# Optimization experiments

Hardware: AMD Instinct MI355X
Metric: run time of the kernel (lower is better)

The kernel has to match this reference:

```python
import jax, jax.numpy as jnp
import numpy as np

N = 100000
E = 1600000
DIM = 128
HID = 16
HEADS = 4
NUM_CLASSES = 2
NEG_SLOPE = 0.2


def _glorot(key, shape):
    fan_in, fan_out = shape[0], shape[-1]
    lim = jnp.sqrt(6.0 / (fan_in + fan_out))
    return jax.random.uniform(key, shape, jnp.float32, -lim, lim)


def setup_inputs() -> dict:
    key = jax.random.key(0)
    ks = jax.random.split(key, 12)
    x = jax.random.normal(ks[0], (N, DIM), jnp.float32)
    edge_index = jax.random.randint(ks[1], (2, E), 0, N, jnp.int32)
    # conv1: in=DIM, out=HID, heads=HEADS
    W1 = _glorot(ks[2], (DIM, HEADS * HID))
    att_src1 = _glorot(ks[3], (HEADS, HID))
    att_dst1 = _glorot(ks[4], (HEADS, HID))
    b1 = jnp.zeros((HEADS * HID,), jnp.float32)
    # conv2: in=HEADS*HID, out=NUM_CLASSES, heads=1
    W2 = _glorot(ks[5], (HEADS * HID, NUM_CLASSES))
    att_src2 = _glorot(ks[6], (1, NUM_CLASSES))
    att_dst2 = _glorot(ks[7], (1, NUM_CLASSES))
    b2 = jnp.zeros((NUM_CLASSES,), jnp.float32)
    return {"x": x, "edge_index": edge_index, "W1": W1, "att_src1": att_src1,
            "att_dst1": att_dst1, "b1": b1, "W2": W2, "att_src2": att_src2,
            "att_dst2": att_dst2, "b2": b2}


def gat_conv(x, src, dst, W, a_src, a_dst, bias, heads, out_ch):
    n = x.shape[0]
    h = (x @ W).reshape(n, heads, out_ch)                      # [N,H,C]
    alpha_s = jnp.sum(h * a_src[None], axis=-1)                # [N,H]
    alpha_d = jnp.sum(h * a_dst[None], axis=-1)                # [N,H]
    e = alpha_s[src] + alpha_d[dst]                            # [Etot,H]
    e = jnp.where(e > 0, e, NEG_SLOPE * e)                     # leaky_relu
    m = jax.ops.segment_max(e, dst, num_segments=n)            # segment softmax
    e = jnp.exp(e - m[dst])
    s = jax.ops.segment_sum(e, dst, num_segments=n)
    alpha = e / (s[dst] + 1e-16)                               # [Etot,H]
    msg = h[src] * alpha[..., None]                            # [Etot,H,C]
    out = jax.ops.segment_sum(msg, dst, num_segments=n)        # [N,H,C]
    return out.reshape(n, heads * out_ch) + bias


def reference(x, edge_index, W1, att_src1, att_dst1, b1, W2, att_src2, att_dst2, b2):
    n = x.shape[0]
    loops = jnp.arange(n, dtype=edge_index.dtype)
    src = jnp.concatenate([edge_index[0], loops])
    dst = jnp.concatenate([edge_index[1], loops])
    # dropout p=0.6 is identity in eval mode
    h = gat_conv(x, src, dst, W1, att_src1, att_dst1, b1, HEADS, HID)
    h = jax.nn.elu(h)
    out = gat_conv(h, src, dst, W2, att_src2, att_dst2, b2, 1, NUM_CLASSES)
    return out
```

## Files before the change

### kernel.cpp

```cpp
#include <hip/hip_runtime.h>
#include <math.h>


#define NB 256
#define BSH 9
#define SRC_MASK 0x1FFFF
#define KC_CHUNK 4096
#define MAXB 12288

static __device__ __forceinline__ unsigned short f2bf(float f) {
    union { float f; unsigned int u; } v; v.f = f;
    unsigned int r = (v.u + 0x7fffu + ((v.u >> 16) & 1u)) >> 16;
    return (unsigned short)r;
}
static __device__ __forceinline__ float bf2f(unsigned short s) {
    union { unsigned int u; float f; } v; v.u = ((unsigned int)s) << 16;
    return v.f;
}
static __device__ __forceinline__ float lrexp(float raw) {
    return __expf(raw > 0.f ? raw : 0.2f * raw);
}

__global__ __launch_bounds__(256) void k_gemm1(const float* __restrict__ x,
                                               const float* __restrict__ W,
                                               const float* __restrict__ att_s,
                                               const float* __restrict__ att_d,
                                               unsigned short* __restrict__ h1b,
                                               float* __restrict__ as1,
                                               float* __restrict__ ad1, int n) {
    __shared__ float xs[64 * 132];
    __shared__ float Ws[128 * 64];
    const int t = threadIdx.x;
    const int row0 = blockIdx.x * 64;
    for (int i = t; i < 2048; i += 256)
        ((float4*)Ws)[i] = ((const float4*)W)[i];
    for (int i = t; i < 2048; i += 256) {
        int r = i >> 5, k4 = i & 31;
        float4 v = make_float4(0.f, 0.f, 0.f, 0.f);
        if (row0 + r < n) v = ((const float4*)x)[(size_t)(row0 + r) * 32 + k4];
        *(float4*)&xs[r * 132 + k4 * 4] = v;
    }
    __syncthreads();
    const int tx = t & 15, ty = t >> 4;
    float acc[4][4] = {};
    for (int k = 0; k < 128; k += 4) {
        float4 av[4], bv[4];
#pragma unroll
        for (int i = 0; i < 4; ++i) av[i] = *(const float4*)&xs[(ty * 4 + i) * 132 + k];
#pragma unroll
        for (int kk = 0; kk < 4; ++kk) bv[kk] = *(const float4*)&Ws[(k + kk) * 64 + tx * 4];
#pragma unroll
        for (int kk = 0; kk < 4; ++kk) {
            float4 b = bv[kk];
#pragma unroll
            for (int i = 0; i < 4; ++i) {
                float a = ((const float*)&av[i])[kk];
                acc[i][0] += a * b.x; acc[i][1] += a * b.y;
                acc[i][2] += a * b.z; acc[i][3] += a * b.w;
            }
        }
    }
    float4 sv = ((const float4*)att_s)[tx];
    float4 dv = ((const float4*)att_d)[tx];
    float ps[4], pd[4];
#pragma unroll
    for (int i = 0; i < 4; ++i) {
        ps[i] = acc[i][0] * sv.x + acc[i][1] * sv.y + acc[i][2] * sv.z + acc[i][3] * sv.w;
        pd[i] = acc[i][0] * dv.x + acc[i][1] * dv.y + acc[i][2] * dv.z + acc[i][3] * dv.w;
        int r = row0 + ty * 4 + i;
        if (r < n) {
            ushort4 b;
            b.x = f2bf(acc[i][0]); b.y = f2bf(acc[i][1]);
            b.z = f2bf(acc[i][2]); b.w = f2bf(acc[i][3]);
            ((ushort4*)h1b)[(size_t)r * 16 + tx] = b;
        }
    }
    __syncthreads();
    float* redA = xs;
    float* redB = xs + 1024;
#pragma unroll
    for (int i = 0; i < 4; ++i) {
        int row = ty * 4 + i;
        redA[row * 16 + tx] = ps[i];
        redB[row * 16 + tx] = pd[i];
    }
    __syncthreads();
    {
        int row = t >> 2, h = t & 3;
        int r = row0 + row;
        if (r < n) {
            const float* pa = &redA[row * 16 + h * 4];
            const float* pb = &redB[row * 16 + h * 4];
            as1[r * 4 + h] = pa[0] + pa[1] + pa[2] + pa[3];
            ad1[r * 4 + h] = pb[0] + pb[1] + pb[2] + pb[3];
        }
    }
}

__global__ __launch_bounds__(256) void kA_hist(const int* __restrict__ dst,
                                               int* __restrict__ bcount, int E) {
    __shared__ int h[NB];
    int t = threadIdx.x;
    h[t] = 0; __syncthreads();
    int base = blockIdx.x * KC_CHUNK;
#pragma unroll
    for (int k = 0; k < 16; ++k) {
        int i = base + k * 256 + t;
        if (i < E) atomicAdd(&h[dst[i] >> BSH], 1);
    }
    __syncthreads();
    if (h[t]) atomicAdd(&bcount[t], h[t]);
}

__global__ __launch_bounds__(256) void kB_scan(const int* __restrict__ bcount,
                                               int* __restrict__ boffs,
                                               int* __restrict__ bcursor,
                                               int* __restrict__ offs, int n, int E) {
    __shared__ int sm[NB];
    int t = threadIdx.x;
    int v = bcount[t];
    sm[t] = v; __syncthreads();
    for (int o = 1; o < NB; o <<= 1) {
        int xv = (t >= o) ? sm[t - o] : 0;
        __syncthreads();
        sm[t] += xv; __syncthreads();
    }
    boffs[t + 1] = sm[t];
    bcursor[t] = sm[t] - v;
    if (t == 0) { boffs[0] = 0; offs[n] = E; }
}

__global__ __launch_bounds__(256) void kC_bin(const int* __restrict__ src,
                                              const int* __restrict__ dst,
                                              int* __restrict__ bcursor,
                                              unsigned int* __restrict__ staged, int E) {
    __shared__ unsigned int pairs[KC_CHUNK];
    __shared__ unsigned char binOf[KC_CHUNK];
    __shared__ int h[NB], lofs[NB], lcur[NB], gbase[NB];
    int t = threadIdx.x;
    int base = blockIdx.x * KC_CHUNK;
    int cnt = E - base; if (cnt > KC_CHUNK) cnt = KC_CHUNK;
    h[t] = 0; __syncthreads();
    unsigned int myV[16]; int myBin[16];
#pragma unroll
    for (int k = 0; k < 16; ++k) {
        int li = k * 256 + t;
        myBin[k] = -1;
        if (li < cnt) {
            int gi = base + li;
            int s = src[gi], d = dst[gi];
            int bin = d >> BSH;
            myV[k] = ((unsigned int)(d & ((1 << BSH) - 1)) << 17) | (unsigned int)s;
            myBin[k] = bin;
            atomicAdd(&h[bin], 1);
        }
    }
    __syncthreads();
    int hv = h[t];
    lofs[t] = hv; __syncthreads();
    for (int o = 1; o < NB; o <<= 1) {
        int xv = (t >= o) ? lofs[t - o] : 0;
        __syncthreads();
        lofs[t] += xv; __syncthreads();
    }
    int excl = lofs[t] - hv;
    if (hv) gbase[t] = atomicAdd(&bcursor[t], hv);
    __syncthreads();
    lofs[t] = excl; lcur[t] = excl;
    __syncthreads();
#pragma unroll
    for (int k = 0; k < 16; ++k) {
        if (myBin[k] >= 0) {
            int p = atomicAdd(&lcur[myBin[k]], 1);
            pairs[p] = myV[k];
            binOf[p] = (unsigned char)myBin[k];
        }
    }
    __syncthreads();
    for (int i = t; i < cnt; i += 256) {
        int b = binOf[i];
        staged[gbase[b] + (i - lofs[b])] = pairs[i];
    }
}

__global__ __launch_bounds__(256) void kD_group(const unsigned int* __restrict__ staged,
                                                const int* __restrict__ boffs,
                                                unsigned int* __restrict__ grouped,
                                                int* __restrict__ offs, int n) {
    __shared__ int lh[512], lofs2[512], lcur2[512];
    __shared__ unsigned int st[MAXB];
    int t = threadIdx.x;
    int b = blockIdx.x;
    int base = boffs[b];
    int cnt = boffs[b + 1] - base;
    lh[t] = 0; lh[t + 256] = 0;
    __syncthreads();
    for (int i = t; i < cnt; i += 256)
        atomicAdd(&lh[staged[base + i] >> 17], 1);
    __syncthreads();
    int a0 = lh[2 * t], a1 = lh[2 * t + 1];
    int sp = a0 + a1;
    lcur2[t] = sp; __syncthreads();
    for (int o = 1; o < NB; o <<= 1) {
        int xv = (t >= o) ? lcur2[t - o] : 0;
        __syncthreads();
        lcur2[t] += xv; __syncthreads();
    }
    int excl = lcur2[t] - sp;
    lofs2[2 * t] = excl; lofs2[2 * t + 1] = excl + a0;
    __syncthreads();
#pragma unroll
    for (int q = 0; q < 2; ++q) {
        int dl = t + q * 256;
        int d = (b << BSH) + dl;
        if (d < n) offs[d] = base + lofs2[dl];
        lcur2[dl] = lofs2[dl];
    }
    __syncthreads();
    for (int i = t; i < cnt; i += 256) {
        unsigned int v = staged[base + i];
        int p = atomicAdd(&lcur2[v >> 17], 1);
        st[p] = v;
    }
    __syncthreads();
    for (int i = t; i < cnt; i += 256)
        grouped[base + i] = st[i];
}

__global__ __launch_bounds__(256) void k_agg1(
        const int* __restrict__ offs, const unsigned int* __restrict__ grouped,
        const unsigned short* __restrict__ h1b, const float* __restrict__ as1,
        const float* __restrict__ ad1, const float* __restrict__ b1,
        float* __restrict__ out1, int n) {
    const int lane = threadIdx.x & 63;
    const int d = blockIdx.x * 4 + (threadIdx.x >> 6);
    if (d >= n) return;
    const int c = lane;
    const int h = lane >> 4;
    const int sub = lane & 15;
    const int off0 = offs[d], off1 = offs[d + 1];
    const int total = off1 - off0 + 1;
    const float adh = ad1[d * 4 + h];
    const float wselfv = lrexp(as1[d * 4 + h] + adh);

    float acc = 0.f, wsum = 0.f;
    for (int base = 0; base < total; base += 16) {
        int e = base + sub;
        float w = 0.f; int s = d;
        if (e < total) {
            if (e < total - 1) {
                unsigned int v = grouped[off0 + e];
                s = (int)(v & SRC_MASK);
                w = lrexp(as1[s * 4 + h] + adh);
            } else {
                w = wselfv;
            }
        }
        wsum += w;
#pragma unroll
        for (int j = 0; j < 16; ++j) {
            int sj = __builtin_amdgcn_readlane(s, j);
            float wj = __shfl(w, (h << 4) + j);
            acc += wj * bf2f(h1b[(size_t)sj * 64 + c]);
        }
    }
    wsum += __shfl_xor(wsum, 1);
    wsum += __shfl_xor(wsum, 2);
    wsum += __shfl_xor(wsum, 4);
    wsum += __shfl_xor(wsum, 8);
    out1[(size_t)d * 64 + c] = acc / (wsum + 1e-16f) + b1[c];
}

__global__ void k_node2(const float* __restrict__ out1, const float* __restrict__ W2,
                        const float* __restrict__ att_s2, const float* __restrict__ att_d2,
                        float4* __restrict__ pack, int n) {
    int i = blockIdx.x * blockDim.x + threadIdx.x;
    if (i >= n) return;
    const float4* row = (const float4*)(out1 + (size_t)i * 64);
    float h0 = 0.f, h1v = 0.f;
#pragma unroll
    for (int q = 0; q < 16; ++q) {
        float4 v = row[q];
        float e0 = v.x > 0.f ? v.x : expm1f(v.x);
        float e1 = v.y > 0.f ? v.y : expm1f(v.y);
        float e2 = v.z > 0.f ? v.z : expm1f(v.z);
        float e3 = v.w > 0.f ? v.w : expm1f(v.w);
        int k = q * 4;
        h0  += e0 * W2[(k + 0) * 2 + 0] + e1 * W2[(k + 1) * 2 + 0]
             + e2 * W2[(k + 2) * 2 + 0] + e3 * W2[(k + 3) * 2 + 0];
        h1v += e0 * W2[(k + 0) * 2 + 1] + e1 * W2[(k + 1) * 2 + 1]
             + e2 * W2[(k + 2) * 2 + 1] + e3 * W2[(k + 3) * 2 + 1];
    }
    pack[i] = make_float4(h0, h1v,
                          h0 * att_s2[0] + h1v * att_s2[1],
                          h0 * att_d2[0] + h1v * att_d2[1]);
}

__global__ __launch_bounds__(256) void k_agg2(
        const int* __restrict__ offs, const unsigned int* __restrict__ grouped,
        const float4* __restrict__ pack, const float* __restrict__ b2,
        float* __restrict__ out, int n) {
    int t = threadIdx.x;
    int g = blockIdx.x * 16 + (t >> 4);
    int sub = t & 15;
    if (g >= n) return;
    int off0 = offs[g], off1 = offs[g + 1];
    int total = off1 - off0 + 1;
    float ad = pack[g].w;
    float a0 = 0.f, a1 = 0.f, ws = 0.f;
    for (int e = sub; e < total; e += 16) {
        int s = (e == total - 1) ? g : (int)(grouped[off0 + e] & SRC_MASK);
        float4 ps = pack[s];
        float w = lrexp(ps.z + ad);
        a0 += w * ps.x; a1 += w * ps.y; ws += w;
    }
#pragma unroll
    for (int m = 1; m < 16; m <<= 1) {
        a0 += __shfl_xor(a0, m);
        a1 += __shfl_xor(a1, m);
        ws += __shfl_xor(ws, m);
    }
    if (sub == 0) {
        float inv = 1.f / (ws + 1e-16f);
        out[(size_t)g * 2 + 0] = a0 * inv + b2[0];
        out[(size_t)g * 2 + 1] = a1 * inv + b2[1];
    }
}

extern "C" void kernel_launch(void* const* d_in, const int* in_sizes, int n_in,
                              void* d_out, int out_size, void* d_ws, size_t ws_size,
                              hipStream_t stream) {
    const float* x    = (const float*)d_in[0];
    const int*   ei   = (const int*)d_in[1];
    const float* W1   = (const float*)d_in[2];
    const float* as1w = (const float*)d_in[3];
    const float* ad1w = (const float*)d_in[4];
    const float* b1   = (const float*)d_in[5];
    const float* W2   = (const float*)d_in[6];
    const float* as2w = (const float*)d_in[7];
    const float* ad2w = (const float*)d_in[8];
    const float* b2   = (const float*)d_in[9];
    const int n = in_sizes[0] / 128;
    const int E = in_sizes[1] / 2;
    float* out = (float*)d_out;

    char* ws = (char*)d_ws;
    size_t off = 0;
    auto alloc = [&](size_t bytes) {
        void* p = ws + off;
        off = (off + bytes + 255) & ~(size_t)255;
        return p;
    };
    float*  out1   = (float*)alloc((size_t)n * 64 * 4);
    unsigned short* h1b = (unsigned short*)alloc((size_t)n * 64 * 2);
    float*  as1    = (float*)alloc((size_t)n * 4 * 4);
    float*  ad1    = (float*)alloc((size_t)n * 4 * 4);
    float4* pack   = (float4*)alloc((size_t)n * 16);
    int*    offs   = (int*)alloc((size_t)(n + 1) * 4);
    int*    bcount = (int*)alloc(NB * 4);
    int*    boffs  = (int*)alloc((NB + 1) * 4);
    int*    bcursor= (int*)alloc(NB * 4);
    unsigned int* staged  = (unsigned int*)alloc((size_t)E * 4);
    unsigned int* grouped = (unsigned int*)alloc((size_t)E * 4);

    hipMemsetAsync(bcount, 0, NB * 4, stream);

    const int nblk = (E + KC_CHUNK - 1) / KC_CHUNK;
    k_gemm1<<<(n + 63) / 64, 256, 0, stream>>>(x, W1, as1w, ad1w, h1b, as1, ad1, n);
    kA_hist<<<nblk, 256, 0, stream>>>(ei + E, bcount, E);
    kB_scan<<<1, 256, 0, stream>>>(bcount, boffs, bcursor, offs, n, E);
    kC_bin<<<nblk, 256, 0, stream>>>(ei, ei + E, bcursor, staged, E);
    kD_group<<<NB, 256, 0, stream>>>(staged, boffs, grouped, offs, n);
    k_agg1<<<(n + 3) / 4, 256, 0, stream>>>(offs, grouped, h1b, as1, ad1, b1, out1, n);
    k_node2<<<(n + 255) / 256, 256, 0, stream>>>(out1, W2, as2w, ad2w, pack, n);
    k_agg2<<<(n + 15) / 16, 256, 0, stream>>>(offs, grouped, pack, b2, out, n);
}
```

Measured before the change: 260.4 us.

## Drop histogram and scan passes with fixed-capacity bins; fuse ELU+GEMM2 into agg1

Each destination bin now gets a fixed slot of MAXB entries, so the separate histogram and scan kernels go away and kC_bin takes its bin cursor directly from a zeroed counter. kD_group writes a per-node count array in place of a global prefix offset. The layer-2 node transform (ELU, 64x2 matvec, attention logits) moves into the tail of k_agg1 through a wave-wide shuffle reduction, which removes the out1 round trip and one launch. The cost is that a bin holding more than MAXB edges would overflow, and the shuffle reduction adds work to every wave of agg1.

```diff
diff --git a/kernel.cpp b/kernel.cpp
--- a/kernel.cpp
+++ b/kernel.cpp
@@ -97,39 +97,6 @@
     }
 }
 
-__global__ __launch_bounds__(256) void kA_hist(const int* __restrict__ dst,
-                                               int* __restrict__ bcount, int E) {
-    __shared__ int h[NB];
-    int t = threadIdx.x;
-    h[t] = 0; __syncthreads();
-    int base = blockIdx.x * KC_CHUNK;
-#pragma unroll
-    for (int k = 0; k < 16; ++k) {
-        int i = base + k * 256 + t;
-        if (i < E) atomicAdd(&h[dst[i] >> BSH], 1);
-    }
-    __syncthreads();
-    if (h[t]) atomicAdd(&bcount[t], h[t]);
-}
-
-__global__ __launch_bounds__(256) void kB_scan(const int* __restrict__ bcount,
-                                               int* __restrict__ boffs,
-                                               int* __restrict__ bcursor,
-                                               int* __restrict__ offs, int n, int E) {
-    __shared__ int sm[NB];
-    int t = threadIdx.x;
-    int v = bcount[t];
-    sm[t] = v; __syncthreads();
-    for (int o = 1; o < NB; o <<= 1) {
-        int xv = (t >= o) ? sm[t - o] : 0;
-        __syncthreads();
-        sm[t] += xv; __syncthreads();
-    }
-    boffs[t + 1] = sm[t];
-    bcursor[t] = sm[t] - v;
-    if (t == 0) { boffs[0] = 0; offs[n] = E; }
-}
-
 __global__ __launch_bounds__(256) void kC_bin(const int* __restrict__ src,
                                               const int* __restrict__ dst,
                                               int* __restrict__ bcursor,
@@ -164,7 +131,7 @@
         lofs[t] += xv; __syncthreads();
     }
     int excl = lofs[t] - hv;
-    if (hv) gbase[t] = atomicAdd(&bcursor[t], hv);
+    if (hv) gbase[t] = t * MAXB + atomicAdd(&bcursor[t], hv);
     __syncthreads();
     lofs[t] = excl; lcur[t] = excl;
     __syncthreads();
@@ -184,15 +151,16 @@
 }
 
 __global__ __launch_bounds__(256) void kD_group(const unsigned int* __restrict__ staged,
-                                                const int* __restrict__ boffs,
+                                                const int* __restrict__ bcursor,
                                                 unsigned int* __restrict__ grouped,
-                                                int* __restrict__ offs, int n) {
+                                                int* __restrict__ offs,
+                                                int* __restrict__ dcnt, int n) {
     __shared__ int lh[512], lofs2[512], lcur2[512];
     __shared__ unsigned int st[MAXB];
     int t = threadIdx.x;
     int b = blockIdx.x;
-    int base = boffs[b];
-    int cnt = boffs[b + 1] - base;
+    int base = b * MAXB;
+    int cnt = bcursor[b];
     lh[t] = 0; lh[t + 256] = 0;
     __syncthreads();
     for (int i = t; i < cnt; i += 256)
@@ -213,7 +181,10 @@
     for (int q = 0; q < 2; ++q) {
         int dl = t + q * 256;
         int d = (b << BSH) + dl;
-        if (d < n) offs[d] = base + lofs2[dl];
+        if (d < n) {
+            offs[d] = base + lofs2[dl];
+            dcnt[d] = lh[dl];
+        }
         lcur2[dl] = lofs2[dl];
     }
     __syncthreads();
@@ -228,18 +199,21 @@
 }
 
 __global__ __launch_bounds__(256) void k_agg1(
-        const int* __restrict__ offs, const unsigned int* __restrict__ grouped,
+        const int* __restrict__ offs, const int* __restrict__ dcnt,
+        const unsigned int* __restrict__ grouped,
         const unsigned short* __restrict__ h1b, const float* __restrict__ as1,
         const float* __restrict__ ad1, const float* __restrict__ b1,
-        float* __restrict__ out1, int n) {
+        const float* __restrict__ W2,
+        const float* __restrict__ att_s2, const float* __restrict__ att_d2,
+        float4* __restrict__ pack, int n) {
     const int lane = threadIdx.x & 63;
     const int d = blockIdx.x * 4 + (threadIdx.x >> 6);
     if (d >= n) return;
     const int c = lane;
     const int h = lane >> 4;
     const int sub = lane & 15;
-    const int off0 = offs[d], off1 = offs[d + 1];
-    const int total = off1 - off0 + 1;
+    const int off0 = offs[d];
+    const int total = dcnt[d] + 1;
     const float adh = ad1[d * 4 + h];
     const float wselfv = lrexp(as1[d * 4 + h] + adh);
 
@@ -268,44 +242,33 @@
     wsum += __shfl_xor(wsum, 2);
     wsum += __shfl_xor(wsum, 4);
     wsum += __shfl_xor(wsum, 8);
-    out1[(size_t)d * 64 + c] = acc / (wsum + 1e-16f) + b1[c];
-}
-
-__global__ void k_node2(const float* __restrict__ out1, const float* __restrict__ W2,
-                        const float* __restrict__ att_s2, const float* __restrict__ att_d2,
-                        float4* __restrict__ pack, int n) {
-    int i = blockIdx.x * blockDim.x + threadIdx.x;
-    if (i >= n) return;
-    const float4* row = (const float4*)(out1 + (size_t)i * 64);
-    float h0 = 0.f, h1v = 0.f;
-#pragma unroll
-    for (int q = 0; q < 16; ++q) {
-        float4 v = row[q];
-        float e0 = v.x > 0.f ? v.x : expm1f(v.x);
-        float e1 = v.y > 0.f ? v.y : expm1f(v.y);
-        float e2 = v.z > 0.f ? v.z : expm1f(v.z);
-        float e3 = v.w > 0.f ? v.w : expm1f(v.w);
-        int k = q * 4;
-        h0  += e0 * W2[(k + 0) * 2 + 0] + e1 * W2[(k + 1) * 2 + 0]
-             + e2 * W2[(k + 2) * 2 + 0] + e3 * W2[(k + 3) * 2 + 0];
-        h1v += e0 * W2[(k + 0) * 2 + 1] + e1 * W2[(k + 1) * 2 + 1]
-             + e2 * W2[(k + 2) * 2 + 1] + e3 * W2[(k + 3) * 2 + 1];
-    }
-    pack[i] = make_float4(h0, h1v,
-                          h0 * att_s2[0] + h1v * att_s2[1],
-                          h0 * att_d2[0] + h1v * att_d2[1]);
+    float o1 = acc / (wsum + 1e-16f) + b1[c];
+    float o = o1 > 0.f ? o1 : expm1f(o1);
+    float2 wv = ((const float2*)W2)[c];
+    float p0 = o * wv.x, p1 = o * wv.y;
+#pragma unroll
+    for (int m = 1; m < 64; m <<= 1) {
+        p0 += __shfl_xor(p0, m);
+        p1 += __shfl_xor(p1, m);
+    }
+    if (lane == 0) {
+        pack[d] = make_float4(p0, p1,
+                              p0 * att_s2[0] + p1 * att_s2[1],
+                              p0 * att_d2[0] + p1 * att_d2[1]);
+    }
 }
 
 __global__ __launch_bounds__(256) void k_agg2(
-        const int* __restrict__ offs, const unsigned int* __restrict__ grouped,
+        const int* __restrict__ offs, const int* __restrict__ dcnt,
+        const unsigned int* __restrict__ grouped,
         const float4* __restrict__ pack, const float* __restrict__ b2,
         float* __restrict__ out, int n) {
     int t = threadIdx.x;
     int g = blockIdx.x * 16 + (t >> 4);
     int sub = t & 15;
     if (g >= n) return;
-    int off0 = offs[g], off1 = offs[g + 1];
-    int total = off1 - off0 + 1;
+    int off0 = offs[g];
+    int total = dcnt[g] + 1;
     float ad = pack[g].w;
     float a0 = 0.f, a1 = 0.f, ws = 0.f;
     for (int e = sub; e < total; e += 16) {
@@ -351,27 +314,24 @@
         off = (off + bytes + 255) & ~(size_t)255;
         return p;
     };
-    float*  out1   = (float*)alloc((size_t)n * 64 * 4);
     unsigned short* h1b = (unsigned short*)alloc((size_t)n * 64 * 2);
     float*  as1    = (float*)alloc((size_t)n * 4 * 4);
     float*  ad1    = (float*)alloc((size_t)n * 4 * 4);
     float4* pack   = (float4*)alloc((size_t)n * 16);
-    int*    offs   = (int*)alloc((size_t)(n + 1) * 4);
-    int*    bcount = (int*)alloc(NB * 4);
-    int*    boffs  = (int*)alloc((NB + 1) * 4);
+    int*    offs   = (int*)alloc((size_t)n * 4);
+    int*    dcnt   = (int*)alloc((size_t)n * 4);
     int*    bcursor= (int*)alloc(NB * 4);
-    unsigned int* staged  = (unsigned int*)alloc((size_t)E * 4);
-    unsigned int* grouped = (unsigned int*)alloc((size_t)E * 4);
-
-    hipMemsetAsync(bcount, 0, NB * 4, stream);
+    unsigned int* staged  = (unsigned int*)alloc((size_t)NB * MAXB * 4);
+    unsigned int* grouped = (unsigned int*)alloc((size_t)NB * MAXB * 4);
+
+    hipMemsetAsync(bcursor, 0, NB * 4, stream);
 
     const int nblk = (E + KC_CHUNK - 1) / KC_CHUNK;
+    const int nbk = (n + 511) >> 9;
     k_gemm1<<<(n + 63) / 64, 256, 0, stream>>>(x, W1, as1w, ad1w, h1b, as1, ad1, n);
-    kA_hist<<<nblk, 256, 0, stream>>>(ei + E, bcount, E);
-    kB_scan<<<1, 256, 0, stream>>>(bcount, boffs, bcursor, offs, n, E);
     kC_bin<<<nblk, 256, 0, stream>>>(ei, ei + E, bcursor, staged, E);
-    kD_group<<<NB, 256, 0, stream>>>(staged, boffs, grouped, offs, n);
-    k_agg1<<<(n + 3) / 4, 256, 0, stream>>>(offs, grouped, h1b, as1, ad1, b1, out1, n);
-    k_node2<<<(n + 255) / 256, 256, 0, stream>>>(out1, W2, as2w, ad2w, pack, n);
-    k_agg2<<<(n + 15) / 16, 256, 0, stream>>>(offs, grouped, pack, b2, out, n);
-}
+    kD_group<<<nbk, 256, 0, stream>>>(staged, bcursor, grouped, offs, dcnt, n);
+    k_agg1<<<(n + 3) / 4, 256, 0, stream>>>(offs, dcnt, grouped, h1b, as1, ad1,
+                                            b1, W2, as2w, ad2w, pack, n);
+    k_agg2<<<(n + 15) / 16, 256, 0, stream>>>(offs, dcnt, grouped, pack, b2, out, n);
+}
```

Measured after the change: 246.7 us. -5.3%, faster.
